# Performance work log

Measured on AMD Instinct MI355X. Metric: run time of the kernel, lower is better.

## Reference

```python
import jax, jax.numpy as jnp
import numpy as np

N = 100000
E = 1600000
D = 128
H = 128


def gcn_conv(x, W, b, src, dst, n_nodes):
    # x: [N, Din] -> linear transform first (PyG GCNConv)
    h = x @ W  # [N, Dout]
    # add self loops
    loop = jnp.arange(n_nodes, dtype=src.dtype)
    s = jnp.concatenate([src, loop])
    d = jnp.concatenate([dst, loop])
    # symmetric normalization: deg computed on destination (col) with unit weights
    deg = jnp.zeros((n_nodes,), dtype=h.dtype).at[d].add(1.0)
    dinv = jnp.where(deg > 0, jax.lax.rsqrt(deg), 0.0)
    norm = dinv[s] * dinv[d]  # [E+N]
    msg = h[s] * norm[:, None]  # gather + scale
    out = jax.ops.segment_sum(msg, d, num_segments=n_nodes)
    return out + b


def setup_inputs() -> dict:
    key = jax.random.key(0)
    ks = jax.random.split(key, 8)
    x = jax.random.normal(ks[0], (N, D), dtype=jnp.float32)
    edge_index = jax.random.randint(ks[1], (2, E), 0, N, dtype=jnp.int32)
    sc = 1.0 / np.sqrt(D)
    gate_W = jax.random.uniform(ks[2], (D, D), jnp.float32, -sc, sc)
    gate_b = jax.random.uniform(ks[3], (D,), jnp.float32, -sc, sc)
    W1 = jax.random.normal(ks[4], (D, H), dtype=jnp.float32) * sc
    b1 = jnp.zeros((H,), jnp.float32)
    W2 = jax.random.normal(ks[5], (H, H), dtype=jnp.float32) * (1.0 / np.sqrt(H))
    b2 = jnp.zeros((H,), jnp.float32)
    return {"x": x, "edge_index": edge_index, "gate_W": gate_W, "gate_b": gate_b,
            "W1": W1, "b1": b1, "W2": W2, "b2": b2}


def reference(x, edge_index, gate_W, gate_b, W1, b1, W2, b2):
    src, dst = edge_index[0], edge_index[1]
    gate = jax.nn.sigmoid(x @ gate_W + gate_b)
    h = x * gate
    h = gcn_conv(h, W1, b1, src, dst, N)
    h = jax.nn.relu(h)
    h = gcn_conv(h, W2, b2, src, dst, N)
    return h
```

## Files before the change

### kernel.cpp

```cpp
#include <hip/hip_runtime.h>
#include <hip/hip_bf16.h>
#include <math.h>


#define BUCKET_SHIFT 8
#define BUCKET_W 256
#define CAP 4864
#define NB_MAX 512
#define OSTRIDE 136

typedef __attribute__((ext_vector_type(8))) short bf16x8;
typedef __attribute__((ext_vector_type(4))) float f32x4;

__device__ __forceinline__ unsigned short f2bf(float x) {
    unsigned int u = __float_as_uint(x);
    unsigned int r = (u + 0x7FFFu + ((u >> 16) & 1u)) >> 16;
    return (unsigned short)r;
}
__device__ __forceinline__ float blo(unsigned int u) { return __uint_as_float(u << 16); }
__device__ __forceinline__ float bhi(unsigned int u) { return __uint_as_float(u & 0xFFFF0000u); }

__device__ __forceinline__ void cvt_hilo8(const float* v, bf16x8& hi, bf16x8& lo) {
#pragma unroll
    for (int j = 0; j < 8; j++) {
        unsigned short h = f2bf(v[j]);
        float hf = __uint_as_float((unsigned int)h << 16);
        hi[j] = (short)h;
        lo[j] = (short)f2bf(v[j] - hf);
    }
}

__device__ __forceinline__ f32x4 MF(bf16x8 a, bf16x8 b, f32x4 c) {
    return __builtin_amdgcn_mfma_f32_16x16x32_bf16(a, b, c, 0, 0, 0);
}

__global__ __launch_bounds__(512)
void prepinit_kernel(const float* __restrict__ W0, const float* __restrict__ W1,
                     const float* __restrict__ W2, uint4* __restrict__ img,
                     int* __restrict__ bcursor, int NB) {
    int b = blockIdx.x, t = threadIdx.x;
    if (b < 12) {
        int idx = b * 512 + t;
        int c = idx & 127, kb = (idx >> 7) & 15, w = idx >> 11;
        const float* W = (w == 0) ? W0 : (w == 1) ? W1 : W2;
        bf16x8 hb;
#pragma unroll
        for (int j = 0; j < 8; j++) hb[j] = (short)f2bf(W[(size_t)(kb * 8 + j) * 128 + c]);
        img[w * 2048 + c * 16 + (kb ^ (c & 15))] = *(uint4*)&hb;
    } else {
        if (t < NB) bcursor[t] = 0;
    }
}

__device__ __forceinline__ void partition_body(char* smem, int b, int t,
                                               const int* __restrict__ src,
                                               const int* __restrict__ dst,
                                               int* __restrict__ bucketCursor,
                                               unsigned int* __restrict__ part,
                                               int E, int NB, int chunk) {
    int* hist  = (int*)smem;
    int* basec = hist + NB_MAX;
    int e0 = b * chunk;
    int e1 = min(E, e0 + chunk);

    for (int i = t; i < NB; i += 512) hist[i] = 0;
    __syncthreads();
    for (int e = e0 + t; e < e1; e += 512) {
        int bb = dst[e] >> BUCKET_SHIFT;
        atomicAdd(&hist[bb], 1);
    }
    __syncthreads();
    for (int i = t; i < NB; i += 512) {
        int c = hist[i];
        basec[i] = c ? atomicAdd(&bucketCursor[i], c) : 0;
    }
    __syncthreads();
    for (int i = t; i < NB; i += 512) hist[i] = 0;
    __syncthreads();
    for (int e = e0 + t; e < e1; e += 512) {
        int d = dst[e], s = src[e];
        int bb = d >> BUCKET_SHIFT;
        int r = atomicAdd(&hist[bb], 1);
        int pos = basec[bb] + r;
        if (pos < CAP)
            part[(size_t)bb * CAP + pos] = ((unsigned int)(d & (BUCKET_W - 1)) << 17) | (unsigned int)s;
    }
}

__device__ __forceinline__ void gate_body(char* smem, int gb, int t,
                                          const float* __restrict__ x,
                                          const uint4* __restrict__ gimg,
                                          const float* __restrict__ gate_b,
                                          unsigned short* __restrict__ hpack, int n) {
    uint4* Wl = (uint4*)smem;
    unsigned short* OutS = (unsigned short*)(smem + 32768);
    int lane = t & 63, wv = t >> 6;
    int blockRow = gb * 128;

    for (int idx = t; idx < 2048; idx += 512) Wl[idx] = gimg[idx];

    bf16x8 Ahi[4], Alo[4];
    {
        int arow = blockRow + wv * 16 + (lane & 15);
        const float* ap = x + (size_t)min(arow, n - 1) * 128 + (lane >> 4) * 8;
#pragma unroll
        for (int s = 0; s < 4; s++) {
            float v[8];
            *(float4*)&v[0] = *(const float4*)&ap[s * 32];
            *(float4*)&v[4] = *(const float4*)&ap[s * 32 + 4];
            cvt_hilo8(v, Ahi[s], Alo[s]);
        }
    }
    __syncthreads();

    f32x4 acc[8];
#pragma unroll
    for (int nt = 0; nt < 8; nt++) acc[nt] = (f32x4)(0.f);
#pragma unroll
    for (int s = 0; s < 4; s++) {
        int kb = s * 4 + (lane >> 4);
#pragma unroll
        for (int nt = 0; nt < 8; nt++) {
            int c = nt * 16 + (lane & 15);
            bf16x8 bh = *(bf16x8*)&Wl[c * 16 + (kb ^ (lane & 15))];
            acc[nt] = MF(Ahi[s], bh, acc[nt]);
            acc[nt] = MF(Alo[s], bh, acc[nt]);
        }
    }

    int rl0 = wv * 16 + (lane >> 4) * 4;
#pragma unroll
    for (int nt = 0; nt < 8; nt++) {
        int c = nt * 16 + (lane & 15);
        float gb2 = gate_b[c];
#pragma unroll
        for (int r = 0; r < 4; r++) {
            int grow = min(blockRow + rl0 + r, n - 1);
            float xv = x[(size_t)grow * 128 + c];
            float hv = xv / (1.f + __expf(-(acc[nt][r] + gb2)));
            OutS[(rl0 + r) * OSTRIDE + c] = f2bf(hv);
        }
    }
    __syncthreads();
    {
        int row = t >> 2;
        int c0 = (t & 3) * 32;
        int grow = blockRow + row;
        if (grow < n) {
#pragma unroll
            for (int j = 0; j < 4; j++) {
                uint4 v = *(uint4*)&OutS[row * OSTRIDE + c0 + j * 8];
                *(uint4*)&hpack[(size_t)grow * 128 + c0 + j * 8] = v;
            }
        }
    }
}

__global__ __launch_bounds__(512)
void pg_kernel(const int* __restrict__ src, const int* __restrict__ dst,
               int* __restrict__ bucketCursor, unsigned int* __restrict__ part,
               int E, int NB, int chunk,
               const float* __restrict__ x, const uint4* __restrict__ gimg,
               const float* __restrict__ gate_b, unsigned short* __restrict__ hpack, int n) {
    __shared__ __align__(16) char smem[67584];
    int b = blockIdx.x, t = threadIdx.x;
    if (b < 256) partition_body(smem, b, t, src, dst, bucketCursor, part, E, NB, chunk);
    else         gate_body(smem, b - 256, t, x, gimg, gate_b, hpack, n);
}

__global__ __launch_bounds__(512)
void scan_deg_kernel(const unsigned int* __restrict__ part,
                     const int* __restrict__ bucketCursor,
                     int* __restrict__ bucketBase, float* __restrict__ dinv,
                     int NB, int N) {
    __shared__ int sm[NB_MAX];
    int b = blockIdx.x, t = threadIdx.x;
    if (b < NB) {
        int* deg = sm;
        if (t < 256) deg[t] = 0;
        __syncthreads();
        int cnt = min(bucketCursor[b], CAP);
        for (int i = t; i < cnt; i += 512)
            atomicAdd(&deg[part[(size_t)b * CAP + i] >> 17], 1);
        __syncthreads();
        if (t < 256) {
            int gnode = b * BUCKET_W + t;
            if (gnode < N) dinv[gnode] = rsqrtf((float)(deg[t] + 1));
        }
    } else {
        int v = (t < NB) ? min(bucketCursor[t], CAP) : 0;
        sm[t] = v;
        __syncthreads();
        for (int off = 1; off < NB_MAX; off <<= 1) {
            int a = (t >= off) ? sm[t - off] : 0;
            __syncthreads();
            sm[t] += a;
            __syncthreads();
        }
        if (t < NB) bucketBase[t + 1] = sm[t];
        if (t == 0) bucketBase[0] = 0;
    }
}

__device__ __forceinline__ void fill_body(char* smem, int b, int t,
                                          const unsigned int* __restrict__ part,
                                          const int* __restrict__ bucketBase,
                                          int* __restrict__ rowptr,
                                          int* __restrict__ col, int N, int NB) {
    unsigned int* eLDS = (unsigned int*)smem;
    int* deg  = (int*)(smem + CAP * 4);
    int* cur  = deg + BUCKET_W;
    int* wsum = cur + BUCKET_W;

    int base = bucketBase[b];
    int cnt = bucketBase[b + 1] - base;

    for (int i = t; i < cnt; i += 512) eLDS[i] = part[(size_t)b * CAP + i];
    if (t < 256) deg[t] = 0;
    __syncthreads();
    for (int i = t; i < cnt; i += 512) atomicAdd(&deg[eLDS[i] >> 17], 1);
    __syncthreads();

    int v = (t < 256) ? deg[t] : 0;
    int incl = v;
    int lane = t & 63, w = t >> 6;
    for (int off = 1; off < 64; off <<= 1) {
        int u = __shfl_up(incl, off, 64);
        if (lane >= off) incl += u;
    }
    if (lane == 63) wsum[w] = incl;
    __syncthreads();
    int add = 0;
#pragma unroll
    for (int j = 0; j < 4; j++) if (j < w) add += wsum[j];
    int excl = add + incl - v;
    if (t < 256) {
        cur[t] = excl;
        int gnode = b * BUCKET_W + t;
        if (gnode < N) rowptr[gnode] = base + excl;
    }
    if (b == NB - 1 && t == 0) rowptr[N] = base + cnt;
    __syncthreads();

    for (int i = t; i < cnt; i += 512) {
        unsigned int ev = eLDS[i];
        int dl = ev >> 17;
        int p = atomicAdd(&cur[dl], 1);
        col[base + p] = (int)(ev & 0x1FFFFu);
    }
}

__device__ __forceinline__ void gemm_body(char* smem, int gb, int t,
                                          const unsigned short* __restrict__ A,
                                          const uint4* __restrict__ wimg,
                                          const float* __restrict__ dinv,
                                          unsigned short* __restrict__ g, int n) {
    uint4* Wl = (uint4*)smem;
    unsigned short* OutS = (unsigned short*)(smem + 32768);
    int lane = t & 63, wv = t >> 6;
    int blockRow = gb * 128;

    for (int idx = t; idx < 2048; idx += 512) Wl[idx] = wimg[idx];

    bf16x8 Af[4];
    {
        int arow = blockRow + wv * 16 + (lane & 15);
        const uint4* ap = (const uint4*)(A + (size_t)min(arow, n - 1) * 128);
#pragma unroll
        for (int s = 0; s < 4; s++) {
            uint4 u = ap[(lane >> 4) + s * 4];
            Af[s] = *(bf16x8*)&u;
        }
    }
    __syncthreads();

    f32x4 acc[8];
#pragma unroll
    for (int nt = 0; nt < 8; nt++) acc[nt] = (f32x4)(0.f);
#pragma unroll
    for (int s = 0; s < 4; s++) {
        int kb = s * 4 + (lane >> 4);
#pragma unroll
        for (int nt = 0; nt < 8; nt++) {
            int c = nt * 16 + (lane & 15);
            bf16x8 bh = *(bf16x8*)&Wl[c * 16 + (kb ^ (lane & 15))];
            acc[nt] = MF(Af[s], bh, acc[nt]);
        }
    }

    int rl0 = wv * 16 + (lane >> 4) * 4;
    float di[4];
#pragma unroll
    for (int r = 0; r < 4; r++) di[r] = dinv[min(blockRow + rl0 + r, n - 1)];
#pragma unroll
    for (int nt = 0; nt < 8; nt++) {
        int c = nt * 16 + (lane & 15);
#pragma unroll
        for (int r = 0; r < 4; r++)
            OutS[(rl0 + r) * OSTRIDE + c] = f2bf(acc[nt][r] * di[r]);
    }
    __syncthreads();
    {
        int row = t >> 2;
        int c0 = (t & 3) * 32;
        int grow = blockRow + row;
        if (grow < n) {
#pragma unroll
            for (int j = 0; j < 4; j++) {
                uint4 v = *(uint4*)&OutS[row * OSTRIDE + c0 + j * 8];
                *(uint4*)&g[(size_t)grow * 128 + c0 + j * 8] = v;
            }
        }
    }
}

__global__ __launch_bounds__(512)
void fg_kernel(const unsigned int* __restrict__ part, const int* __restrict__ bucketBase,
               int* __restrict__ rowptr, const float* __restrict__ dinv,
               int* __restrict__ col, int N, int NB,
               const unsigned short* __restrict__ A, const uint4* __restrict__ wimg,
               unsigned short* __restrict__ g) {
    __shared__ __align__(16) char smem[67584];
    int b = blockIdx.x, t = threadIdx.x;
    if (b < NB) fill_body(smem, b, t, part, bucketBase, rowptr, col, N, NB);
    else        gemm_body(smem, b - NB, t, A, wimg, dinv, g, N);
}

__global__ __launch_bounds__(256)
void spmm_gemm_kernel(const uint4* __restrict__ g16, const int* __restrict__ rowptr,
                      const int* __restrict__ col, const float* __restrict__ dinv,
                      const float* __restrict__ b1, const uint4* __restrict__ w2img,
                      unsigned short* __restrict__ g2, int n) {
    __shared__ __align__(16) char smem[16896];
    uint4* Hl = (uint4*)smem;
    unsigned short* OutS = (unsigned short*)(smem + 8192);

    int t = threadIdx.x;
    int blockRow = blockIdx.x * 32;

    int r = t >> 3, l = t & 7;
    int i = min(blockRow + r, n - 1);
    float di = dinv[i];

    float acc[16];
    {
        uint4 s0 = g16[(size_t)i * 16 + l];
        uint4 s1 = g16[(size_t)i * 16 + 8 + l];
        acc[0] = blo(s0.x);  acc[1] = bhi(s0.x);
        acc[2] = blo(s0.y);  acc[3] = bhi(s0.y);
        acc[4] = blo(s0.z);  acc[5] = bhi(s0.z);
        acc[6] = blo(s0.w);  acc[7] = bhi(s0.w);
        acc[8] = blo(s1.x);  acc[9] = bhi(s1.x);
        acc[10] = blo(s1.y); acc[11] = bhi(s1.y);
        acc[12] = blo(s1.z); acc[13] = bhi(s1.z);
        acc[14] = blo(s1.w); acc[15] = bhi(s1.w);
    }
    int e0 = rowptr[i], e1 = rowptr[i + 1];
    int e = e0;
    for (; e + 4 <= e1; e += 4) {
        int s0 = col[e], s1 = col[e + 1], s2 = col[e + 2], s3 = col[e + 3];
        uint4 a0 = g16[(size_t)s0 * 16 + l];
        uint4 a1 = g16[(size_t)s0 * 16 + 8 + l];
        uint4 c0 = g16[(size_t)s1 * 16 + l];
        uint4 c1 = g16[(size_t)s1 * 16 + 8 + l];
        uint4 d0 = g16[(size_t)s2 * 16 + l];
        uint4 d1 = g16[(size_t)s2 * 16 + 8 + l];
        uint4 f0 = g16[(size_t)s3 * 16 + l];
        uint4 f1 = g16[(size_t)s3 * 16 + 8 + l];
        acc[0]  += (blo(a0.x) + blo(c0.x)) + (blo(d0.x) + blo(f0.x));
        acc[1]  += (bhi(a0.x) + bhi(c0.x)) + (bhi(d0.x) + bhi(f0.x));
        acc[2]  += (blo(a0.y) + blo(c0.y)) + (blo(d0.y) + blo(f0.y));
        acc[3]  += (bhi(a0.y) + bhi(c0.y)) + (bhi(d0.y) + bhi(f0.y));
        acc[4]  += (blo(a0.z) + blo(c0.z)) + (blo(d0.z) + blo(f0.z));
        acc[5]  += (bhi(a0.z) + bhi(c0.z)) + (bhi(d0.z) + bhi(f0.z));
        acc[6]  += (blo(a0.w) + blo(c0.w)) + (blo(d0.w) + blo(f0.w));
        acc[7]  += (bhi(a0.w) + bhi(c0.w)) + (bhi(d0.w) + bhi(f0.w));
        acc[8]  += (blo(a1.x) + blo(c1.x)) + (blo(d1.x) + blo(f1.x));
        acc[9]  += (bhi(a1.x) + bhi(c1.x)) + (bhi(d1.x) + bhi(f1.x));
        acc[10] += (blo(a1.y) + blo(c1.y)) + (blo(d1.y) + blo(f1.y));
        acc[11] += (bhi(a1.y) + bhi(c1.y)) + (bhi(d1.y) + bhi(f1.y));
        acc[12] += (blo(a1.z) + blo(c1.z)) + (blo(d1.z) + blo(f1.z));
        acc[13] += (bhi(a1.z) + bhi(c1.z)) + (bhi(d1.z) + bhi(f1.z));
        acc[14] += (blo(a1.w) + blo(c1.w)) + (blo(d1.w) + blo(f1.w));
        acc[15] += (bhi(a1.w) + bhi(c1.w)) + (bhi(d1.w) + bhi(f1.w));
    }
    for (; e < e1; e++) {
        int s0 = col[e];
        uint4 a0 = g16[(size_t)s0 * 16 + l];
        uint4 a1 = g16[(size_t)s0 * 16 + 8 + l];
        acc[0]  += blo(a0.x);  acc[1]  += bhi(a0.x);
        acc[2]  += blo(a0.y);  acc[3]  += bhi(a0.y);
        acc[4]  += blo(a0.z);  acc[5]  += bhi(a0.z);
        acc[6]  += blo(a0.w);  acc[7]  += bhi(a0.w);
        acc[8]  += blo(a1.x);  acc[9]  += bhi(a1.x);
        acc[10] += blo(a1.y);  acc[11] += bhi(a1.y);
        acc[12] += blo(a1.z);  acc[13] += bhi(a1.z);
        acc[14] += blo(a1.w);  acc[15] += bhi(a1.w);
    }

    {
        const float* bp0 = b1 + l * 8;
        const float* bp1 = b1 + 64 + l * 8;
        float4 b00 = *(const float4*)&bp0[0], b01 = *(const float4*)&bp0[4];
        float4 b10 = *(const float4*)&bp1[0], b11 = *(const float4*)&bp1[4];
        float h[16];
        h[0] = fmaxf(fmaf(acc[0], di, b00.x), 0.f);
        h[1] = fmaxf(fmaf(acc[1], di, b00.y), 0.f);
        h[2] = fmaxf(fmaf(acc[2], di, b00.z), 0.f);
        h[3] = fmaxf(fmaf(acc[3], di, b00.w), 0.f);
        h[4] = fmaxf(fmaf(acc[4], di, b01.x), 0.f);
        h[5] = fmaxf(fmaf(acc[5], di, b01.y), 0.f);
        h[6] = fmaxf(fmaf(acc[6], di, b01.z), 0.f);
        h[7] = fmaxf(fmaf(acc[7], di, b01.w), 0.f);
        h[8] = fmaxf(fmaf(acc[8], di, b10.x), 0.f);
        h[9] = fmaxf(fmaf(acc[9], di, b10.y), 0.f);
        h[10] = fmaxf(fmaf(acc[10], di, b10.z), 0.f);
        h[11] = fmaxf(fmaf(acc[11], di, b10.w), 0.f);
        h[12] = fmaxf(fmaf(acc[12], di, b11.x), 0.f);
        h[13] = fmaxf(fmaf(acc[13], di, b11.y), 0.f);
        h[14] = fmaxf(fmaf(acc[14], di, b11.z), 0.f);
        h[15] = fmaxf(fmaf(acc[15], di, b11.w), 0.f);
        uint4 p0, p1;
        p0.x = (unsigned int)f2bf(h[0]) | ((unsigned int)f2bf(h[1]) << 16);
        p0.y = (unsigned int)f2bf(h[2]) | ((unsigned int)f2bf(h[3]) << 16);
        p0.z = (unsigned int)f2bf(h[4]) | ((unsigned int)f2bf(h[5]) << 16);
        p0.w = (unsigned int)f2bf(h[6]) | ((unsigned int)f2bf(h[7]) << 16);
        p1.x = (unsigned int)f2bf(h[8]) | ((unsigned int)f2bf(h[9]) << 16);
        p1.y = (unsigned int)f2bf(h[10]) | ((unsigned int)f2bf(h[11]) << 16);
        p1.z = (unsigned int)f2bf(h[12]) | ((unsigned int)f2bf(h[13]) << 16);
        p1.w = (unsigned int)f2bf(h[14]) | ((unsigned int)f2bf(h[15]) << 16);
        int sw = r & 15;
        Hl[r * 16 + (l ^ sw)] = p0;
        Hl[r * 16 + ((l + 8) ^ sw)] = p1;
    }
    __syncthreads();

    int lane = t & 63, wv = t >> 6;
    int rt = wv & 1, ch = wv >> 1;
    bf16x8 Af[4];
    {
        int arow = rt * 16 + (lane & 15);
        int asw = arow & 15;
#pragma unroll
        for (int s = 0; s < 4; s++) {
            int kb = s * 4 + (lane >> 4);
            uint4 u = Hl[arow * 16 + (kb ^ asw)];
            Af[s] = *(bf16x8*)&u;
        }
    }
    f32x4 acc2[4];
#pragma unroll
    for (int ntl = 0; ntl < 4; ntl++) acc2[ntl] = (f32x4)(0.f);
#pragma unroll
    for (int s = 0; s < 4; s++) {
        int kb = s * 4 + (lane >> 4);
#pragma unroll
        for (int ntl = 0; ntl < 4; ntl++) {
            int c = (ch * 4 + ntl) * 16 + (lane & 15);
            uint4 u = w2img[c * 16 + (kb ^ (lane & 15))];
            acc2[ntl] = MF(Af[s], *(bf16x8*)&u, acc2[ntl]);
        }
    }

    int rl0 = rt * 16 + (lane >> 4) * 4;
    float dr[4];
#pragma unroll
    for (int rr = 0; rr < 4; rr++) dr[rr] = dinv[min(blockRow + rl0 + rr, n - 1)];
#pragma unroll
    for (int ntl = 0; ntl < 4; ntl++) {
        int c = (ch * 4 + ntl) * 16 + (lane & 15);
#pragma unroll
        for (int rr = 0; rr < 4; rr++)
            OutS[(rl0 + rr) * OSTRIDE + c] = f2bf(acc2[ntl][rr] * dr[rr]);
    }
    __syncthreads();
    {
        int grow = blockRow + r;
        if (grow < n) {
            uint4 v0 = *(uint4*)&OutS[r * OSTRIDE + l * 16];
            uint4 v1 = *(uint4*)&OutS[r * OSTRIDE + l * 16 + 8];
            *(uint4*)&g2[(size_t)grow * 128 + l * 16] = v0;
            *(uint4*)&g2[(size_t)grow * 128 + l * 16 + 8] = v1;
        }
    }
}

__global__ void spmm_kernel(const uint4* __restrict__ g16, const int* __restrict__ rowptr,
                            const int* __restrict__ col, const float* __restrict__ dinv,
                            const float* __restrict__ bias, float* __restrict__ outv,
                            int n, int nhb) {
    int half = (blockIdx.x >= nhb) ? 1 : 0;
    int rb = blockIdx.x - half * nhb;
    int i = rb * 32 + (threadIdx.x >> 3);
    if (i >= n) return;
    int c = threadIdx.x & 7;

    const uint4* gp = g16 + half * 8 + c;
    float acc[8];
    uint4 sv = gp[(size_t)i * 16];
    acc[0] = blo(sv.x); acc[1] = bhi(sv.x);
    acc[2] = blo(sv.y); acc[3] = bhi(sv.y);
    acc[4] = blo(sv.z); acc[5] = bhi(sv.z);
    acc[6] = blo(sv.w); acc[7] = bhi(sv.w);

    int e0 = rowptr[i], e1 = rowptr[i + 1];
    int e = e0;
    for (; e + 8 <= e1; e += 8) {
        uint4 v0 = gp[(size_t)col[e] * 16];
        uint4 v1 = gp[(size_t)col[e + 1] * 16];
        uint4 v2 = gp[(size_t)col[e + 2] * 16];
        uint4 v3 = gp[(size_t)col[e + 3] * 16];
        uint4 v4 = gp[(size_t)col[e + 4] * 16];
        uint4 v5 = gp[(size_t)col[e + 5] * 16];
        uint4 v6 = gp[(size_t)col[e + 6] * 16];
        uint4 v7 = gp[(size_t)col[e + 7] * 16];
        acc[0] += ((blo(v0.x) + blo(v1.x)) + (blo(v2.x) + blo(v3.x))) +
                  ((blo(v4.x) + blo(v5.x)) + (blo(v6.x) + blo(v7.x)));
        acc[1] += ((bhi(v0.x) + bhi(v1.x)) + (bhi(v2.x) + bhi(v3.x))) +
                  ((bhi(v4.x) + bhi(v5.x)) + (bhi(v6.x) + bhi(v7.x)));
        acc[2] += ((blo(v0.y) + blo(v1.y)) + (blo(v2.y) + blo(v3.y))) +
                  ((blo(v4.y) + blo(v5.y)) + (blo(v6.y) + blo(v7.y)));
        acc[3] += ((bhi(v0.y) + bhi(v1.y)) + (bhi(v2.y) + bhi(v3.y))) +
                  ((bhi(v4.y) + bhi(v5.y)) + (bhi(v6.y) + bhi(v7.y)));
        acc[4] += ((blo(v0.z) + blo(v1.z)) + (blo(v2.z) + blo(v3.z))) +
                  ((blo(v4.z) + blo(v5.z)) + (blo(v6.z) + blo(v7.z)));
        acc[5] += ((bhi(v0.z) + bhi(v1.z)) + (bhi(v2.z) + bhi(v3.z))) +
                  ((bhi(v4.z) + bhi(v5.z)) + (bhi(v6.z) + bhi(v7.z)));
        acc[6] += ((blo(v0.w) + blo(v1.w)) + (blo(v2.w) + blo(v3.w))) +
                  ((blo(v4.w) + blo(v5.w)) + (blo(v6.w) + blo(v7.w)));
        acc[7] += ((bhi(v0.w) + bhi(v1.w)) + (bhi(v2.w) + bhi(v3.w))) +
                  ((bhi(v4.w) + bhi(v5.w)) + (bhi(v6.w) + bhi(v7.w)));
    }
    for (; e + 2 <= e1; e += 2) {
        uint4 v0 = gp[(size_t)col[e] * 16];
        uint4 v1 = gp[(size_t)col[e + 1] * 16];
        acc[0] += blo(v0.x) + blo(v1.x); acc[1] += bhi(v0.x) + bhi(v1.x);
        acc[2] += blo(v0.y) + blo(v1.y); acc[3] += bhi(v0.y) + bhi(v1.y);
        acc[4] += blo(v0.z) + blo(v1.z); acc[5] += bhi(v0.z) + bhi(v1.z);
        acc[6] += blo(v0.w) + blo(v1.w); acc[7] += bhi(v0.w) + bhi(v1.w);
    }
    if (e < e1) {
        uint4 v0 = gp[(size_t)col[e] * 16];
        acc[0] += blo(v0.x); acc[1] += bhi(v0.x);
        acc[2] += blo(v0.y); acc[3] += bhi(v0.y);
        acc[4] += blo(v0.z); acc[5] += bhi(v0.z);
        acc[6] += blo(v0.w); acc[7] += bhi(v0.w);
    }

    float di = dinv[i];
    const float4* b4 = (const float4*)(bias + half * 64);
    float4 bv0 = b4[c * 2], bv1 = b4[c * 2 + 1];
    float r0[8];
    r0[0] = fmaf(acc[0], di, bv0.x);
    r0[1] = fmaf(acc[1], di, bv0.y);
    r0[2] = fmaf(acc[2], di, bv0.z);
    r0[3] = fmaf(acc[3], di, bv0.w);
    r0[4] = fmaf(acc[4], di, bv1.x);
    r0[5] = fmaf(acc[5], di, bv1.y);
    r0[6] = fmaf(acc[6], di, bv1.z);
    r0[7] = fmaf(acc[7], di, bv1.w);
    float* o = outv + (size_t)i * 128 + half * 64 + c * 8;
    f32x4 a = *(f32x4*)&r0[0];
    f32x4 b = *(f32x4*)&r0[4];
    __builtin_nontemporal_store(a, (f32x4*)o);
    __builtin_nontemporal_store(b, (f32x4*)(o + 4));
}

extern "C" void kernel_launch(void* const* d_in, const int* in_sizes, int n_in,
                              void* d_out, int out_size, void* d_ws, size_t ws_size,
                              hipStream_t stream) {
    const float* x      = (const float*)d_in[0];
    const int*   ei     = (const int*)d_in[1];
    const float* gate_W = (const float*)d_in[2];
    const float* gate_b = (const float*)d_in[3];
    const float* W1     = (const float*)d_in[4];
    const float* b1     = (const float*)d_in[5];
    const float* W2     = (const float*)d_in[6];
    const float* b2     = (const float*)d_in[7];
    float* out = (float*)d_out;

    const int N = in_sizes[0] / 128;
    const int E = in_sizes[1] / 2;
    const int* src = ei;
    const int* dst = ei + E;
    const int NB = (N + BUCKET_W - 1) / BUCKET_W;

    char* p = (char*)d_ws;
    auto alloc = [&](size_t bytes) { char* q = p; p += (bytes + 255) & ~(size_t)255; return q; };
    int*   rowptr  = (int*)alloc(((size_t)N + 1) * 4);
    float* dinv    = (float*)alloc((size_t)N * 4);
    int*   colb    = (int*)alloc((size_t)E * 4);
    int*   bcursor = (int*)alloc((size_t)NB * 4);
    int*   bbase   = (int*)alloc(((size_t)NB + 1) * 4);
    uint4* wimg    = (uint4*)alloc((size_t)3 * 2048 * 16);
    unsigned int*   part   = (unsigned int*)alloc((size_t)NB * CAP * 4);
    unsigned short* hpack  = (unsigned short*)alloc((size_t)N * 128 * 2);
    unsigned short* g16    = (unsigned short*)alloc((size_t)N * 128 * 2);
    unsigned short* g2buf  = (unsigned short*)alloc((size_t)N * 128 * 2);

    const int pblocks = 256;
    const int chunk = (E + pblocks - 1) / pblocks;
    int gblocks = (N + 127) / 128;
    int fblocks = (N + 31) / 32;
    int nhb = (N + 31) / 32;

    prepinit_kernel<<<13, 512, 0, stream>>>(gate_W, W1, W2, wimg, bcursor, NB);
    pg_kernel<<<256 + gblocks, 512, 0, stream>>>(src, dst, bcursor, part, E, NB, chunk,
                                                 x, wimg, gate_b, hpack, N);
    scan_deg_kernel<<<NB + 1, 512, 0, stream>>>(part, bcursor, bbase, dinv, NB, N);
    fg_kernel<<<NB + gblocks, 512, 0, stream>>>(part, bbase, rowptr, dinv, colb, N, NB,
                                                hpack, wimg + 2048, g16);
    spmm_gemm_kernel<<<fblocks, 256, 0, stream>>>((const uint4*)g16, rowptr, colb,
                                                  dinv, b1, wimg + 4096, g2buf, N);
    spmm_kernel<<<2 * nhb, 256, 0, stream>>>((const uint4*)g2buf, rowptr, colb,
                                             dinv, b2, out, N, nhb);
}
```

Before: 212.1 us.

## Process SpMM rows in degree-sorted order via counting-sort permutation

Builds a per-node degree histogram during the degree pass, scans it in descending order, and makes a counting-sort permutation of nodes by in-degree inside the fill/gemm kernel. Both SpMM kernels then walk rows through this permutation, so wavefronts and blocks handle nodes of similar degree and lose less time to load imbalance and divergence. The cost is an extra small kernel launch, the histogram atomics, and scattered (non-contiguous) row reads and writes through perm, which hurts locality.

```diff
diff --git a/kernel.cpp b/kernel.cpp
--- a/kernel.cpp
+++ b/kernel.cpp
@@ -37,7 +37,7 @@
 __global__ __launch_bounds__(512)
 void prepinit_kernel(const float* __restrict__ W0, const float* __restrict__ W1,
                      const float* __restrict__ W2, uint4* __restrict__ img,
-                     int* __restrict__ bcursor, int NB) {
+                     int* __restrict__ bcursor, int* __restrict__ hist, int NB) {
     int b = blockIdx.x, t = threadIdx.x;
     if (b < 12) {
         int idx = b * 512 + t;
@@ -47,8 +47,10 @@
 #pragma unroll
         for (int j = 0; j < 8; j++) hb[j] = (short)f2bf(W[(size_t)(kb * 8 + j) * 128 + c]);
         img[w * 2048 + c * 16 + (kb ^ (c & 15))] = *(uint4*)&hb;
+    } else if (b == 12) {
+        if (t < NB) bcursor[t] = 0;
     } else {
-        if (t < NB) bcursor[t] = 0;
+        if (t < 256) hist[t] = 0;
     }
 }
 
@@ -172,12 +174,14 @@
 void scan_deg_kernel(const unsigned int* __restrict__ part,
                      const int* __restrict__ bucketCursor,
                      int* __restrict__ bucketBase, float* __restrict__ dinv,
+                     int* __restrict__ degv, int* __restrict__ hist,
                      int NB, int N) {
     __shared__ int sm[NB_MAX];
     int b = blockIdx.x, t = threadIdx.x;
     if (b < NB) {
-        int* deg = sm;
-        if (t < 256) deg[t] = 0;
+        int* deg  = sm;
+        int* hbin = sm + 256;
+        if (t < 256) { deg[t] = 0; hbin[t] = 0; }
         __syncthreads();
         int cnt = min(bucketCursor[b], CAP);
         for (int i = t; i < cnt; i += 512)
@@ -185,8 +189,15 @@
         __syncthreads();
         if (t < 256) {
             int gnode = b * BUCKET_W + t;
-            if (gnode < N) dinv[gnode] = rsqrtf((float)(deg[t] + 1));
-        }
+            if (gnode < N) {
+                int d = deg[t];
+                dinv[gnode] = rsqrtf((float)(d + 1));
+                degv[gnode] = d;
+                atomicAdd(&hbin[min(d, 255)], 1);
+            }
+        }
+        __syncthreads();
+        if (t < 256 && hbin[t] > 0) atomicAdd(&hist[t], hbin[t]);
     } else {
         int v = (t < NB) ? min(bucketCursor[t], CAP) : 0;
         sm[t] = v;
@@ -202,6 +213,21 @@
     }
 }
 
+__global__ __launch_bounds__(256)
+void histscan_kernel(const int* __restrict__ hist, int* __restrict__ hbase) {
+    __shared__ int sm[256];
+    int t = threadIdx.x;
+    sm[t] = hist[255 - t];
+    __syncthreads();
+    for (int off = 1; off < 256; off <<= 1) {
+        int a = (t >= off) ? sm[t - off] : 0;
+        __syncthreads();
+        sm[t] += a;
+        __syncthreads();
+    }
+    hbase[255 - t] = sm[t] - hist[255 - t];
+}
+
 __device__ __forceinline__ void fill_body(char* smem, int b, int t,
                                           const unsigned int* __restrict__ part,
                                           const int* __restrict__ bucketBase,
@@ -314,23 +340,53 @@
     }
 }
 
+__device__ __forceinline__ void perm_body(char* smem, int pb, int t,
+                                          const int* __restrict__ degv,
+                                          int* __restrict__ hbase,
+                                          int* __restrict__ perm, int N) {
+    int* h2 = (int*)smem;
+    int* bl = h2 + 256;
+    int idx = pb * 512 + t;
+    int bin = -1;
+    if (t < 256) { h2[t] = 0; }
+    __syncthreads();
+    if (idx < N) {
+        bin = min(degv[idx], 255);
+        atomicAdd(&h2[bin], 1);
+    }
+    __syncthreads();
+    if (t < 256) {
+        int c = h2[t];
+        bl[t] = c ? atomicAdd(&hbase[t], c) : 0;
+        h2[t] = 0;
+    }
+    __syncthreads();
+    if (idx < N) {
+        int r = atomicAdd(&h2[bin], 1);
+        perm[bl[bin] + r] = idx;
+    }
+}
+
 __global__ __launch_bounds__(512)
 void fg_kernel(const unsigned int* __restrict__ part, const int* __restrict__ bucketBase,
                int* __restrict__ rowptr, const float* __restrict__ dinv,
-               int* __restrict__ col, int N, int NB,
+               int* __restrict__ col, int N, int NB, int gblocks,
                const unsigned short* __restrict__ A, const uint4* __restrict__ wimg,
-               unsigned short* __restrict__ g) {
+               unsigned short* __restrict__ g,
+               const int* __restrict__ degv, int* __restrict__ hbase,
+               int* __restrict__ perm) {
     __shared__ __align__(16) char smem[67584];
     int b = blockIdx.x, t = threadIdx.x;
-    if (b < NB) fill_body(smem, b, t, part, bucketBase, rowptr, col, N, NB);
-    else        gemm_body(smem, b - NB, t, A, wimg, dinv, g, N);
+    if (b < NB)                fill_body(smem, b, t, part, bucketBase, rowptr, col, N, NB);
+    else if (b < NB + gblocks) gemm_body(smem, b - NB, t, A, wimg, dinv, g, N);
+    else                       perm_body(smem, b - NB - gblocks, t, degv, hbase, perm, N);
 }
 
 __global__ __launch_bounds__(256)
 void spmm_gemm_kernel(const uint4* __restrict__ g16, const int* __restrict__ rowptr,
                       const int* __restrict__ col, const float* __restrict__ dinv,
                       const float* __restrict__ b1, const uint4* __restrict__ w2img,
-                      unsigned short* __restrict__ g2, int n) {
+                      const int* __restrict__ perm, unsigned short* __restrict__ g2, int n) {
     __shared__ __align__(16) char smem[16896];
     uint4* Hl = (uint4*)smem;
     unsigned short* OutS = (unsigned short*)(smem + 8192);
@@ -339,7 +395,7 @@
     int blockRow = blockIdx.x * 32;
 
     int r = t >> 3, l = t & 7;
-    int i = min(blockRow + r, n - 1);
+    int i = perm[min(blockRow + r, n - 1)];
     float di = dinv[i];
 
     float acc[16];
@@ -465,7 +521,8 @@
     int rl0 = rt * 16 + (lane >> 4) * 4;
     float dr[4];
 #pragma unroll
-    for (int rr = 0; rr < 4; rr++) dr[rr] = dinv[min(blockRow + rl0 + rr, n - 1)];
+    for (int rr = 0; rr < 4; rr++)
+        dr[rr] = dinv[perm[min(blockRow + rl0 + rr, n - 1)]];
 #pragma unroll
     for (int ntl = 0; ntl < 4; ntl++) {
         int c = (ch * 4 + ntl) * 16 + (lane & 15);
@@ -477,22 +534,24 @@
     {
         int grow = blockRow + r;
         if (grow < n) {
+            int row = perm[grow];
             uint4 v0 = *(uint4*)&OutS[r * OSTRIDE + l * 16];
             uint4 v1 = *(uint4*)&OutS[r * OSTRIDE + l * 16 + 8];
-            *(uint4*)&g2[(size_t)grow * 128 + l * 16] = v0;
-            *(uint4*)&g2[(size_t)grow * 128 + l * 16 + 8] = v1;
+            *(uint4*)&g2[(size_t)row * 128 + l * 16] = v0;
+            *(uint4*)&g2[(size_t)row * 128 + l * 16 + 8] = v1;
         }
     }
 }
 
 __global__ void spmm_kernel(const uint4* __restrict__ g16, const int* __restrict__ rowptr,
                             const int* __restrict__ col, const float* __restrict__ dinv,
-                            const float* __restrict__ bias, float* __restrict__ outv,
-                            int n, int nhb) {
+                            const float* __restrict__ bias, const int* __restrict__ perm,
+                            float* __restrict__ outv, int n, int nhb) {
     int half = (blockIdx.x >= nhb) ? 1 : 0;
     int rb = blockIdx.x - half * nhb;
-    int i = rb * 32 + (threadIdx.x >> 3);
-    if (i >= n) return;
+    int il = rb * 32 + (threadIdx.x >> 3);
+    if (il >= n) return;
+    int i = perm[il];
     int c = threadIdx.x & 7;
 
     const uint4* gp = g16 + half * 8 + c;
@@ -589,9 +648,13 @@
     auto alloc = [&](size_t bytes) { char* q = p; p += (bytes + 255) & ~(size_t)255; return q; };
     int*   rowptr  = (int*)alloc(((size_t)N + 1) * 4);
     float* dinv    = (float*)alloc((size_t)N * 4);
+    int*   degv    = (int*)alloc((size_t)N * 4);
+    int*   perm    = (int*)alloc((size_t)N * 4);
     int*   colb    = (int*)alloc((size_t)E * 4);
     int*   bcursor = (int*)alloc((size_t)NB * 4);
     int*   bbase   = (int*)alloc(((size_t)NB + 1) * 4);
+    int*   hist    = (int*)alloc(256 * 4);
+    int*   hbase   = (int*)alloc(256 * 4);
     uint4* wimg    = (uint4*)alloc((size_t)3 * 2048 * 16);
     unsigned int*   part   = (unsigned int*)alloc((size_t)NB * CAP * 4);
     unsigned short* hpack  = (unsigned short*)alloc((size_t)N * 128 * 2);
@@ -602,16 +665,20 @@
     const int chunk = (E + pblocks - 1) / pblocks;
     int gblocks = (N + 127) / 128;
     int fblocks = (N + 31) / 32;
+    int permblocks = (N + 511) / 512;
     int nhb = (N + 31) / 32;
 
-    prepinit_kernel<<<13, 512, 0, stream>>>(gate_W, W1, W2, wimg, bcursor, NB);
+    prepinit_kernel<<<14, 512, 0, stream>>>(gate_W, W1, W2, wimg, bcursor, hist, NB);
     pg_kernel<<<256 + gblocks, 512, 0, stream>>>(src, dst, bcursor, part, E, NB, chunk,
                                                  x, wimg, gate_b, hpack, N);
-    scan_deg_kernel<<<NB + 1, 512, 0, stream>>>(part, bcursor, bbase, dinv, NB, N);
-    fg_kernel<<<NB + gblocks, 512, 0, stream>>>(part, bbase, rowptr, dinv, colb, N, NB,
-                                                hpack, wimg + 2048, g16);
+    scan_deg_kernel<<<NB + 1, 512, 0, stream>>>(part, bcursor, bbase, dinv, degv, hist, NB, N);
+    histscan_kernel<<<1, 256, 0, stream>>>(hist, hbase);
+    fg_kernel<<<NB + gblocks + permblocks, 512, 0, stream>>>(part, bbase, rowptr, dinv,
+                                                             colb, N, NB, gblocks,
+                                                             hpack, wimg + 2048, g16,
+                                                             degv, hbase, perm);
     spmm_gemm_kernel<<<fblocks, 256, 0, stream>>>((const uint4*)g16, rowptr, colb,
-                                                  dinv, b1, wimg + 4096, g2buf, N);
+                                                  dinv, b1, wimg + 4096, perm, g2buf, N);
     spmm_kernel<<<2 * nhb, 256, 0, stream>>>((const uint4*)g2buf, rowptr, colb,
-                                             dinv, b2, out, N, nhb);
-}
+                                             dinv, b2, perm, out, N, nhb);
+}
```

Measured after the change: 221.4 us. +4.4%, slower.
